# Optimization experiments

Measured on AMD Instinct MI355X. Metric: run time of the kernel, lower is better.

Reference implementation:

```python
import jax, jax.numpy as jnp
import numpy as np

EMBED = 1024
HEADS = 16
HEAD_DIM = EMBED // HEADS
N, SEQ = 8, 1024


def setup_inputs() -> dict:
    key = jax.random.key(0)
    ks = jax.random.split(key, 9)
    values = jax.random.normal(ks[0], (N, SEQ, EMBED), dtype=jnp.float32)
    keys_ = jax.random.normal(ks[1], (N, SEQ, EMBED), dtype=jnp.float32)
    query = jax.random.normal(ks[2], (N, SEQ, EMBED), dtype=jnp.float32)
    mask = jax.random.randint(ks[3], (N, 1, SEQ, SEQ), 0, 2, dtype=jnp.int32)
    s = 1.0 / np.sqrt(HEAD_DIM)
    Wv = jax.random.normal(ks[4], (HEAD_DIM, HEAD_DIM), dtype=jnp.float32) * s
    Wk = jax.random.normal(ks[5], (HEAD_DIM, HEAD_DIM), dtype=jnp.float32) * s
    Wq = jax.random.normal(ks[6], (HEAD_DIM, HEAD_DIM), dtype=jnp.float32) * s
    Wo = jax.random.normal(ks[7], (EMBED, EMBED), dtype=jnp.float32) * (1.0 / np.sqrt(EMBED))
    bo = jax.random.normal(ks[8], (EMBED,), dtype=jnp.float32) * 0.01
    return {"values": values, "keys": keys_, "query": query, "mask": mask,
            "Wv": Wv, "Wk": Wk, "Wq": Wq, "Wo": Wo, "bo": bo}


def reference(values, keys, query, mask, Wv, Wk, Wq, Wo, bo):
    n, q_len = query.shape[0], query.shape[1]
    v_len, k_len = values.shape[1], keys.shape[1]
    # reshape to (N, len, H, Dh); per-head linear projections share a (Dh,Dh) weight.
    v = values.reshape(n, v_len, HEADS, HEAD_DIM)
    k = keys.reshape(n, k_len, HEADS, HEAD_DIM)
    q = query.reshape(n, q_len, HEADS, HEAD_DIM)
    # torch Linear: x @ W.T
    v = jnp.einsum('nlhd,ed->nlhe', v, Wv)
    k = jnp.einsum('nlhd,ed->nlhe', k, Wk)
    q = jnp.einsum('nlhd,ed->nlhe', q, Wq)
    # scores (N,H,Q,K); mask BEFORE scaling, exactly as the torch module does
    att = jnp.einsum('nqhd,nkhd->nhqk', q, k)
    att = jnp.where(mask == 0, jnp.float32(-1e20), att)
    att = jax.nn.softmax(att / jnp.sqrt(jnp.float32(EMBED)), axis=3)
    out = jnp.einsum('nhql,nlhd->nqhd', att, v).reshape(n, q_len, EMBED)
    return out @ Wo.T + bo
```

## Files before the change

kernel.cpp:

```cpp
#include <hip/hip_runtime.h>
#include <hip/hip_bf16.h>

using bf16x8 = __attribute__((ext_vector_type(8))) __bf16;
using f32x4  = __attribute__((ext_vector_type(4))) float;

#define NB 8
#define SEQ 1024
#define HEADS 16
#define HD 64
#define EMB 1024

#if __has_builtin(__builtin_amdgcn_exp2f)
  #define EXPD(x) __builtin_amdgcn_exp2f(x)
  #define QSCALE  0.04508422f
  #define MASKV  -4.5084e18f
#else
  #define EXPD(x) __expf(x)
  #define QSCALE  0.03125f
  #define MASKV  -3.125e18f
#endif

__global__ __launch_bounds__(256) void mask_pack(const int* __restrict__ mask,
                                                 unsigned long long* __restrict__ mp)
{
    const int row = blockIdx.x, n = blockIdx.y, t = threadIdx.x;
    const int w = t >> 6, lane = t & 63;
    const int* m = mask + ((size_t)n * SEQ + row) * SEQ;
    #pragma unroll
    for (int i = 0; i < 4; ++i) {
        unsigned long long b = __ballot(m[i * 256 + w * 64 + lane] != 0);
        if (lane == 0) mp[((size_t)n * SEQ + row) * 16 + i * 4 + w] = b;
    }
}

__global__ __launch_bounds__(256, 4) void proj_mfma(
    const float* __restrict__ q_in, const float* __restrict__ k_in, const float* __restrict__ v_in,
    const float* __restrict__ Wq, const float* __restrict__ Wk, const float* __restrict__ Wv,
    __bf16* __restrict__ qp, __bf16* __restrict__ kp, __bf16* __restrict__ vpt)
{
    const int z = blockIdx.z;
    const float* X  = (z == 0) ? q_in : (z == 1) ? k_in : v_in;
    const float* Wf = (z == 0) ? Wq   : (z == 1) ? Wk   : Wv;

    __shared__ __align__(16) __bf16 Wb[64 * 72];
    __shared__ __align__(16) __bf16 Xb[64 * 72];
    const int t = threadIdx.x;
    const int nh = blockIdx.y, n = nh >> 4, h = nh & 15;
    const int l0 = blockIdx.x * 64;
    for (int i = t; i < 4096; i += 256)
        Wb[(i >> 6) * 72 + (i & 63)] = (__bf16)Wf[i];
    {
        const int row = t >> 2, seg = (t & 3) * 16;
        const float* src = X + ((size_t)(n * SEQ + l0 + row)) * EMB + h * 64 + seg;
        union { __bf16 b[16]; uint4 u[2]; } tmp;
        #pragma unroll
        for (int jj = 0; jj < 4; ++jj) {
            float4 f = ((const float4*)src)[jj];
            tmp.b[jj*4+0] = (__bf16)f.x; tmp.b[jj*4+1] = (__bf16)f.y;
            tmp.b[jj*4+2] = (__bf16)f.z; tmp.b[jj*4+3] = (__bf16)f.w;
        }
        *(uint4*)&Xb[row * 72 + seg]     = tmp.u[0];
        *(uint4*)&Xb[row * 72 + seg + 8] = tmp.u[1];
    }
    __syncthreads();
    const int w = t >> 6, lane = t & 63, quad = lane >> 4, lr = lane & 15;
    bf16x8 af[2];
    #pragma unroll
    for (int ks = 0; ks < 2; ++ks)
        af[ks] = *(const bf16x8*)&Xb[(w * 16 + lr) * 72 + ks * 32 + quad * 8];
    const f32x4 zero4 = {0.f, 0.f, 0.f, 0.f};
    f32x4 acc[4];
    #pragma unroll
    for (int et = 0; et < 4; ++et) {
        acc[et] = zero4;
        #pragma unroll
        for (int ks = 0; ks < 2; ++ks) {
            bf16x8 bfrag = *(const bf16x8*)&Wb[(et * 16 + lr) * 72 + ks * 32 + quad * 8];
            acc[et] = __builtin_amdgcn_mfma_f32_16x16x32_bf16(af[ks], bfrag, acc[et], 0, 0, 0);
        }
    }
    if (z == 0) {
        #pragma unroll
        for (int et = 0; et < 4; ++et) acc[et] *= QSCALE;
    }
    __syncthreads();
    if (z < 2) {
        #pragma unroll
        for (int et = 0; et < 4; ++et)
            #pragma unroll
            for (int rr = 0; rr < 4; ++rr)
                Xb[(w * 16 + quad * 4 + rr) * 72 + et * 16 + lr] = (__bf16)acc[et][rr];
        __syncthreads();
        const int row = t >> 2, seg = (t & 3) * 16;
        uint4 a = *(uint4*)&Xb[row * 72 + seg];
        uint4 b = *(uint4*)&Xb[row * 72 + seg + 8];
        __bf16* outp = (z == 0) ? qp : kp;
        __bf16* dst = outp + (size_t)nh * 65536 + (size_t)(l0 + row) * 64 + seg;
        *(uint4*)&dst[0] = a;
        *(uint4*)&dst[8] = b;
    } else {
        #pragma unroll
        for (int et = 0; et < 4; ++et)
            #pragma unroll
            for (int rr = 0; rr < 4; ++rr)
                Xb[(et * 16 + lr) * 72 + w * 16 + quad * 4 + rr] = (__bf16)acc[et][rr];
        __syncthreads();
        const int e = t >> 2, seg = (t & 3) * 16;
        uint4 a = *(uint4*)&Xb[e * 72 + seg];
        uint4 b = *(uint4*)&Xb[e * 72 + seg + 8];
        __bf16* dst = vpt + (size_t)nh * 65536 + (size_t)e * SEQ + l0 + seg;
        *(uint4*)&dst[0] = a;
        *(uint4*)&dst[8] = b;
    }
}

__global__ __launch_bounds__(256, 4) void attn_mfma(
    const __bf16* __restrict__ qp, const __bf16* __restrict__ kp, const __bf16* __restrict__ vpt,
    const unsigned long long* __restrict__ mp, __bf16* __restrict__ attn_out)
{
    __shared__ __align__(16) __bf16 Ks[64 * 72];
    __shared__ __align__(16) __bf16 Vt[64 * 72];
    __shared__ __align__(16) __bf16 Ps[4][2][16 * 72];
    const int t = threadIdx.x, w = t >> 6, lane = t & 63, quad = lane >> 4, lr = lane & 15;
    const int bid = blockIdx.x;
    const int nh = bid & 127, qg = bid >> 7;
    const int n = nh >> 4, h = nh & 15;
    const int q0 = qg * 128;
    const __bf16* Q  = qp  + (size_t)nh * 65536;
    const __bf16* K  = kp  + (size_t)nh * 65536;
    const __bf16* VT = vpt + (size_t)nh * 65536;

    int qrow[2];
    bf16x8 qf[2][2];
    const unsigned long long* mrow[2];
    #pragma unroll
    for (int g = 0; g < 2; ++g) {
        qrow[g] = q0 + g * 64 + w * 16 + lr;
        qf[g][0] = *(const bf16x8*)&Q[(size_t)qrow[g] * 64 + quad * 8];
        qf[g][1] = *(const bf16x8*)&Q[(size_t)qrow[g] * 64 + 32 + quad * 8];
        mrow[g] = mp + ((size_t)n * SEQ + qrow[g]) * 16;
    }

    const f32x4 zero4 = {0.f, 0.f, 0.f, 0.f};
    f32x4 O[2][4];
    #pragma unroll
    for (int g = 0; g < 2; ++g)
        #pragma unroll
        for (int mt = 0; mt < 4; ++mt) O[g][mt] = zero4;
    float l_part[2] = {0.f, 0.f};

    for (int kc = 0; kc < 16; ++kc) {
        __syncthreads();
        for (int c = t; c < 512; c += 256) {
            int row = c >> 3, c8 = c & 7;
            *(uint4*)&Ks[row * 72 + c8 * 8] =
                *(const uint4*)&K[(size_t)(kc * 64 + row) * 64 + c8 * 8];
            *(uint4*)&Vt[row * 72 + c8 * 8] =
                *(const uint4*)&VT[(size_t)row * SEQ + kc * 64 + c8 * 8];
        }
        const unsigned long long mw0 = mrow[0][kc], mw1 = mrow[1][kc];
        __syncthreads();
        #pragma unroll
        for (int g = 0; g < 2; ++g) {
            f32x4 S[4];
            #pragma unroll
            for (int kt = 0; kt < 4; ++kt) {
                S[kt] = zero4;
                #pragma unroll
                for (int ks = 0; ks < 2; ++ks) {
                    bf16x8 kf = *(const bf16x8*)&Ks[(kt * 16 + lr) * 72 + ks * 32 + quad * 8];
                    S[kt] = __builtin_amdgcn_mfma_f32_16x16x32_bf16(kf, qf[g][ks], S[kt], 0, 0, 0);
                }
            }
            const unsigned long long mword = g ? mw1 : mw0;
            const unsigned int mlo = (unsigned int)(mword >> (quad * 4));
            const unsigned int mhi = (unsigned int)(mword >> (32 + quad * 4));
            float lsum = 0.f;
            __bf16 pb[16];
            #pragma unroll
            for (int kt = 0; kt < 4; ++kt)
                #pragma unroll
                for (int r = 0; r < 4; ++r) {
                    unsigned int bits = (kt < 2) ? mlo : mhi;
                    int sh = (kt & 1) * 16 + r;
                    float sv = ((bits >> sh) & 1u) ? S[kt][r] : MASKV;
                    float ev = EXPD(sv);
                    lsum += ev;
                    pb[kt * 4 + r] = (__bf16)ev;
                }
            l_part[g] += lsum;
            #pragma unroll
            for (int kt = 0; kt < 4; ++kt) {
                union { __bf16 b[4]; uint2 u; } pk;
                #pragma unroll
                for (int r = 0; r < 4; ++r) pk.b[r] = pb[kt * 4 + r];
                *(uint2*)&Ps[w][g][lr * 72 + kt * 16 + quad * 4] = pk.u;
            }
        }
        __asm__ __volatile__("s_waitcnt lgkmcnt(0)" ::: "memory");
        #pragma unroll
        for (int ks = 0; ks < 2; ++ks) {
            bf16x8 pf0 = *(const bf16x8*)&Ps[w][0][lr * 72 + ks * 32 + quad * 8];
            bf16x8 pf1 = *(const bf16x8*)&Ps[w][1][lr * 72 + ks * 32 + quad * 8];
            #pragma unroll
            for (int mt = 0; mt < 4; ++mt) {
                bf16x8 vf = *(const bf16x8*)&Vt[(mt * 16 + lr) * 72 + ks * 32 + quad * 8];
                O[0][mt] = __builtin_amdgcn_mfma_f32_16x16x32_bf16(vf, pf0, O[0][mt], 0, 0, 0);
                O[1][mt] = __builtin_amdgcn_mfma_f32_16x16x32_bf16(vf, pf1, O[1][mt], 0, 0, 0);
            }
        }
    }
    #pragma unroll
    for (int g = 0; g < 2; ++g) {
        float l = l_part[g];
        l += __shfl_xor(l, 16, 64);
        l += __shfl_xor(l, 32, 64);
        const float linv = 1.0f / l;
        #pragma unroll
        for (int mt = 0; mt < 4; ++mt) {
            union { __bf16 b[4]; uint2 u; } pk;
            #pragma unroll
            for (int r = 0; r < 4; ++r) pk.b[r] = (__bf16)(O[g][mt][r] * linv);
            *(uint2*)&attn_out[((size_t)n * SEQ + qrow[g]) * EMB + h * 64 + mt * 16 + quad * 4] = pk.u;
        }
    }
}

__global__ __launch_bounds__(256) void cvt_wo(const float* __restrict__ Wo, __bf16* __restrict__ Wob)
{
    int i = blockIdx.x * 256 + threadIdx.x;
    float4 f = *(const float4*)&Wo[(size_t)i * 4];
    union { __bf16 b[4]; uint2 u; } tmp;
    tmp.b[0] = (__bf16)f.x; tmp.b[1] = (__bf16)f.y; tmp.b[2] = (__bf16)f.z; tmp.b[3] = (__bf16)f.w;
    *(uint2*)&Wob[(size_t)i * 4] = tmp.u;
}

__global__ __launch_bounds__(256, 4) void out_gemm_mfma(
    const __bf16* __restrict__ A, const __bf16* __restrict__ B,
    const float* __restrict__ bo, float* __restrict__ out)
{
    __shared__ __align__(16) __bf16 As[64 * 40];
    __shared__ __align__(16) __bf16 Bs[128 * 40];
    const int t = threadIdx.x, w = t >> 6, lane = t & 63, quad = lane >> 4, lr = lane & 15;
    const int wr = (w >> 1) * 32, wc = (w & 1) * 64;
    const int r0 = blockIdx.y * 64, e0 = blockIdx.x * 128;
    const f32x4 zero4 = {0.f, 0.f, 0.f, 0.f};
    f32x4 acc[2][4];
    #pragma unroll
    for (int mt = 0; mt < 2; ++mt)
        #pragma unroll
        for (int nt = 0; nt < 4; ++nt) acc[mt][nt] = zero4;
    for (int k0 = 0; k0 < 1024; k0 += 32) {
        __syncthreads();
        {
            int row = t >> 2, c8 = t & 3;
            *(uint4*)&As[row * 40 + c8 * 8] =
                *(const uint4*)&A[(size_t)(r0 + row) * EMB + k0 + c8 * 8];
        }
        for (int c = t; c < 512; c += 256) {
            int row = c >> 2, c8 = c & 3;
            *(uint4*)&Bs[row * 40 + c8 * 8] =
                *(const uint4*)&B[(size_t)(e0 + row) * EMB + k0 + c8 * 8];
        }
        __syncthreads();
        bf16x8 af[2], bf[4];
        #pragma unroll
        for (int mt = 0; mt < 2; ++mt)
            af[mt] = *(const bf16x8*)&As[(wr + mt * 16 + lr) * 40 + quad * 8];
        #pragma unroll
        for (int nt = 0; nt < 4; ++nt)
            bf[nt] = *(const bf16x8*)&Bs[(wc + nt * 16 + lr) * 40 + quad * 8];
        #pragma unroll
        for (int mt = 0; mt < 2; ++mt)
            #pragma unroll
            for (int nt = 0; nt < 4; ++nt)
                acc[mt][nt] = __builtin_amdgcn_mfma_f32_16x16x32_bf16(af[mt], bf[nt], acc[mt][nt], 0, 0, 0);
    }
    float bv[4];
    #pragma unroll
    for (int nt = 0; nt < 4; ++nt) bv[nt] = bo[e0 + wc + nt * 16 + lr];
    #pragma unroll
    for (int mt = 0; mt < 2; ++mt)
        #pragma unroll
        for (int nt = 0; nt < 4; ++nt)
            #pragma unroll
            for (int rr = 0; rr < 4; ++rr)
                out[(size_t)(r0 + wr + mt * 16 + quad * 4 + rr) * EMB + e0 + wc + nt * 16 + lr] =
                    acc[mt][nt][rr] + bv[nt];
}

extern "C" void kernel_launch(void* const* d_in, const int* in_sizes, int n_in,
                              void* d_out, int out_size, void* d_ws, size_t ws_size,
                              hipStream_t stream) {
    const float* values = (const float*)d_in[0];
    const float* keys   = (const float*)d_in[1];
    const float* query  = (const float*)d_in[2];
    const int*   mask   = (const int*)d_in[3];
    const float* Wv     = (const float*)d_in[4];
    const float* Wk     = (const float*)d_in[5];
    const float* Wq     = (const float*)d_in[6];
    const float* Wo     = (const float*)d_in[7];
    const float* bo     = (const float*)d_in[8];
    float* out = (float*)d_out;

    const size_t per = (size_t)NB * HEADS * SEQ * HD;
    __bf16* qp   = (__bf16*)d_ws;
    __bf16* kp   = qp + per;
    __bf16* vpt  = kp + per;
    __bf16* attn = vpt + per;
    __bf16* Wob  = attn + (size_t)NB * SEQ * EMB;
    unsigned long long* maskp = (unsigned long long*)(Wob + (size_t)EMB * EMB);

    mask_pack<<<dim3(SEQ, NB), 256, 0, stream>>>(mask, maskp);
    proj_mfma<<<dim3(16, 128, 3), 256, 0, stream>>>(query, keys, values, Wq, Wk, Wv, qp, kp, vpt);
    cvt_wo<<<1024, 256, 0, stream>>>(Wo, Wob);
    attn_mfma<<<1024, 256, 0, stream>>>(qp, kp, vpt, maskp, attn);
    out_gemm_mfma<<<dim3(EMB / 128, NB * SEQ / 64), 256, 0, stream>>>(attn, Wob, bo, out);
}
```

Measured before the change: 283.1 us.

## Double-buffer swizzled K/V with async LDS loads and keep P in registers

The attention kernel now copies K and V tiles straight from global memory into a double-buffered, XOR-swizzled LDS area using global_load_lds, issuing the next tile before computing the current one. This overlaps loads with compute and drops one barrier per tile. Softmax probabilities are packed with v_cvt_pk_bf16_f32 and rearranged across lanes with permlane swaps, replacing the LDS write/read round trip for P. The QK MFMAs are interleaved across both query groups and wrapped in s_setprio. The changes add correctness risk around LDS address layout and async-load waits.

```diff
diff --git a/kernel.cpp b/kernel.cpp
--- a/kernel.cpp
+++ b/kernel.cpp
@@ -19,6 +19,17 @@
   #define QSCALE  0.03125f
   #define MASKV  -3.125e18f
 #endif
+
+__device__ __forceinline__ int cvtpk_bf16(float lo, float hi) {
+    int r;
+    asm("v_cvt_pk_bf16_f32 %0, %1, %2" : "=v"(r) : "v"(lo), "v"(hi));
+    return r;
+}
+
+__device__ __forceinline__ void gld16(const __bf16* g, __bf16* l) {
+    __builtin_amdgcn_global_load_lds((const __attribute__((address_space(1))) void*)g,
+                                     (__attribute__((address_space(3))) void*)l, 16, 0, 0);
+}
 
 __global__ __launch_bounds__(256) void mask_pack(const int* __restrict__ mask,
                                                  unsigned long long* __restrict__ mp)
@@ -118,9 +129,7 @@
     const __bf16* __restrict__ qp, const __bf16* __restrict__ kp, const __bf16* __restrict__ vpt,
     const unsigned long long* __restrict__ mp, __bf16* __restrict__ attn_out)
 {
-    __shared__ __align__(16) __bf16 Ks[64 * 72];
-    __shared__ __align__(16) __bf16 Vt[64 * 72];
-    __shared__ __align__(16) __bf16 Ps[4][2][16 * 72];
+    __shared__ __align__(16) __bf16 KV[2][2][64 * 64];
     const int t = threadIdx.x, w = t >> 6, lane = t & 63, quad = lane >> 4, lr = lane & 15;
     const int bid = blockIdx.x;
     const int nh = bid & 127, qg = bid >> 7;
@@ -141,6 +150,26 @@
         mrow[g] = mp + ((size_t)n * SEQ + qrow[g]) * 16;
     }
 
+    const int srow = t >> 3, sc8 = t & 7;
+    const int sswz = (sc8 ^ (srow & 7)) * 8;
+    const int kofs = srow * 64 + sswz;
+    const int vofs = srow * SEQ + sswz;
+
+    auto issue = [&](int kc) {
+        const int b = kc & 1;
+        __bf16* kb = (__bf16*)&KV[b][0][0];
+        __bf16* vb = (__bf16*)&KV[b][1][0];
+        const __bf16* ksrc = K  + (size_t)kc * 4096 + kofs;
+        const __bf16* vsrc = VT + (size_t)kc * 64   + vofs;
+        gld16(ksrc,            kb + t * 8);
+        gld16(ksrc + 32 * 64,  kb + t * 8 + 2048);
+        gld16(vsrc,            vb + t * 8);
+        gld16(vsrc + 32 * SEQ, vb + t * 8 + 2048);
+    };
+
+    const int s0 = ((quad ^ (lr & 7))) * 8;
+    const int s1 = s0 ^ 32;
+
     const f32x4 zero4 = {0.f, 0.f, 0.f, 0.f};
     f32x4 O[2][4];
     #pragma unroll
@@ -149,66 +178,80 @@
         for (int mt = 0; mt < 4; ++mt) O[g][mt] = zero4;
     float l_part[2] = {0.f, 0.f};
 
+    issue(0);
     for (int kc = 0; kc < 16; ++kc) {
         __syncthreads();
-        for (int c = t; c < 512; c += 256) {
-            int row = c >> 3, c8 = c & 7;
-            *(uint4*)&Ks[row * 72 + c8 * 8] =
-                *(const uint4*)&K[(size_t)(kc * 64 + row) * 64 + c8 * 8];
-            *(uint4*)&Vt[row * 72 + c8 * 8] =
-                *(const uint4*)&VT[(size_t)row * SEQ + kc * 64 + c8 * 8];
-        }
+        if (kc + 1 < 16) issue(kc + 1);
         const unsigned long long mw0 = mrow[0][kc], mw1 = mrow[1][kc];
-        __syncthreads();
+        const __bf16* Kb = (const __bf16*)&KV[kc & 1][0][0];
+        const __bf16* Vb = (const __bf16*)&KV[kc & 1][1][0];
+
+        f32x4 S[2][4];
+        #pragma unroll
+        for (int g = 0; g < 2; ++g)
+            #pragma unroll
+            for (int kt = 0; kt < 4; ++kt) S[g][kt] = zero4;
+        __builtin_amdgcn_s_setprio(1);
+        #pragma unroll
+        for (int kt = 0; kt < 4; ++kt) {
+            bf16x8 kf0 = *(const bf16x8*)&Kb[(kt * 16 + lr) * 64 + s0];
+            bf16x8 kf1 = *(const bf16x8*)&Kb[(kt * 16 + lr) * 64 + s1];
+            S[0][kt] = __builtin_amdgcn_mfma_f32_16x16x32_bf16(kf0, qf[0][0], S[0][kt], 0, 0, 0);
+            S[1][kt] = __builtin_amdgcn_mfma_f32_16x16x32_bf16(kf0, qf[1][0], S[1][kt], 0, 0, 0);
+            S[0][kt] = __builtin_amdgcn_mfma_f32_16x16x32_bf16(kf1, qf[0][1], S[0][kt], 0, 0, 0);
+            S[1][kt] = __builtin_amdgcn_mfma_f32_16x16x32_bf16(kf1, qf[1][1], S[1][kt], 0, 0, 0);
+        }
+        __builtin_amdgcn_s_setprio(0);
+
+        bf16x8 pf[2][2];
         #pragma unroll
         for (int g = 0; g < 2; ++g) {
-            f32x4 S[4];
-            #pragma unroll
-            for (int kt = 0; kt < 4; ++kt) {
-                S[kt] = zero4;
-                #pragma unroll
-                for (int ks = 0; ks < 2; ++ks) {
-                    bf16x8 kf = *(const bf16x8*)&Ks[(kt * 16 + lr) * 72 + ks * 32 + quad * 8];
-                    S[kt] = __builtin_amdgcn_mfma_f32_16x16x32_bf16(kf, qf[g][ks], S[kt], 0, 0, 0);
-                }
-            }
             const unsigned long long mword = g ? mw1 : mw0;
             const unsigned int mlo = (unsigned int)(mword >> (quad * 4));
             const unsigned int mhi = (unsigned int)(mword >> (32 + quad * 4));
+            float ev[16];
             float lsum = 0.f;
-            __bf16 pb[16];
             #pragma unroll
             for (int kt = 0; kt < 4; ++kt)
                 #pragma unroll
                 for (int r = 0; r < 4; ++r) {
                     unsigned int bits = (kt < 2) ? mlo : mhi;
                     int sh = (kt & 1) * 16 + r;
-                    float sv = ((bits >> sh) & 1u) ? S[kt][r] : MASKV;
-                    float ev = EXPD(sv);
-                    lsum += ev;
-                    pb[kt * 4 + r] = (__bf16)ev;
+                    float sv = ((bits >> sh) & 1u) ? S[g][kt][r] : MASKV;
+                    float e = EXPD(sv);
+                    lsum += e;
+                    ev[kt * 4 + r] = e;
                 }
             l_part[g] += lsum;
             #pragma unroll
-            for (int kt = 0; kt < 4; ++kt) {
-                union { __bf16 b[4]; uint2 u; } pk;
-                #pragma unroll
-                for (int r = 0; r < 4; ++r) pk.b[r] = pb[kt * 4 + r];
-                *(uint2*)&Ps[w][g][lr * 72 + kt * 16 + quad * 4] = pk.u;
+            for (int ks = 0; ks < 2; ++ks) {
+                const int ka = (2 * ks) * 4, kb2 = (2 * ks + 1) * 4;
+                int d0 = cvtpk_bf16(ev[ka + 0], ev[ka + 1]);
+                int d1 = cvtpk_bf16(ev[ka + 2], ev[ka + 3]);
+                int d2 = cvtpk_bf16(ev[kb2 + 0], ev[kb2 + 1]);
+                int d3 = cvtpk_bf16(ev[kb2 + 2], ev[kb2 + 3]);
+                asm("v_permlane32_swap_b32 %0, %1" : "+v"(d0), "+v"(d2));
+                asm("v_permlane16_swap_b32 %0, %1" : "+v"(d0), "+v"(d2));
+                asm("v_permlane32_swap_b32 %0, %1" : "+v"(d1), "+v"(d3));
+                asm("v_permlane16_swap_b32 %0, %1" : "+v"(d1), "+v"(d3));
+                union { int di[4]; bf16x8 v; } pb;
+                pb.di[0] = d0; pb.di[1] = d1; pb.di[2] = d2; pb.di[3] = d3;
+                pf[g][ks] = pb.v;
             }
         }
-        __asm__ __volatile__("s_waitcnt lgkmcnt(0)" ::: "memory");
+
+        __builtin_amdgcn_s_setprio(1);
         #pragma unroll
         for (int ks = 0; ks < 2; ++ks) {
-            bf16x8 pf0 = *(const bf16x8*)&Ps[w][0][lr * 72 + ks * 32 + quad * 8];
-            bf16x8 pf1 = *(const bf16x8*)&Ps[w][1][lr * 72 + ks * 32 + quad * 8];
+            const int sv = ks ? s1 : s0;
             #pragma unroll
             for (int mt = 0; mt < 4; ++mt) {
-                bf16x8 vf = *(const bf16x8*)&Vt[(mt * 16 + lr) * 72 + ks * 32 + quad * 8];
-                O[0][mt] = __builtin_amdgcn_mfma_f32_16x16x32_bf16(vf, pf0, O[0][mt], 0, 0, 0);
-                O[1][mt] = __builtin_amdgcn_mfma_f32_16x16x32_bf16(vf, pf1, O[1][mt], 0, 0, 0);
+                bf16x8 vf = *(const bf16x8*)&Vb[(mt * 16 + lr) * 64 + sv];
+                O[0][mt] = __builtin_amdgcn_mfma_f32_16x16x32_bf16(vf, pf[0][ks], O[0][mt], 0, 0, 0);
+                O[1][mt] = __builtin_amdgcn_mfma_f32_16x16x32_bf16(vf, pf[1][ks], O[1][mt], 0, 0, 0);
             }
         }
+        __builtin_amdgcn_s_setprio(0);
     }
     #pragma unroll
     for (int g = 0; g < 2; ++g) {
```

Result: no change. 278.3 us (-1.7%).
